# Optimization experiments

Hardware: AMD Instinct MI355X
Metric: run time of the kernel (lower is better)

## Reference

```python
import jax, jax.numpy as jnp
import numpy as np

FEATURES = 1024
NUM_REFLECTIONS = 4
BATCH = 65536


def setup_inputs() -> dict:
    key = jax.random.key(0)
    kx, kv = jax.random.split(key)
    x = jax.random.normal(kx, (BATCH, FEATURES), dtype=jnp.float32)
    vectors = jax.random.normal(kv, (NUM_REFLECTIONS, FEATURES), dtype=jnp.float32)
    return {"x": x, "vectors": vectors}


def _construct_orthogonal(vectors):
    n = vectors.shape[-1]
    I = jnp.eye(n, dtype=vectors.dtype)
    Q = I
    # Small fixed loop over reflections (num_reflections is tiny).
    for i in range(vectors.shape[0]):
        v = vectors[i]
        v = v / jnp.linalg.norm(v)  # F.normalize(v, dim=-1)
        H = I - 2.0 * jnp.outer(v, v)
        Q = H @ Q
    return Q


def reference(x, vectors):
    W = _construct_orthogonal(vectors)
    return x @ W.T
```

## Files before the change

kernel.cpp:

```cpp
#include <hip/hip_runtime.h>
#include <hip/hip_bf16.h>

#define FEATURES 1024
#define NREFL 4

__global__ __launch_bounds__(256) void hh_normalize(const float* __restrict__ vec,
                                                    float* __restrict__ w) {
    __shared__ float red[4];
    const int i = blockIdx.x;
    const int t = threadIdx.x;
    const float4 val = *(const float4*)(vec + i * FEATURES + t * 4);
    float s = val.x * val.x + val.y * val.y + val.z * val.z + val.w * val.w;
    #pragma unroll
    for (int off = 32; off > 0; off >>= 1) s += __shfl_xor(s, off);
    if ((t & 63) == 0) red[t >> 6] = s;
    __syncthreads();
    const float total = red[0] + red[1] + red[2] + red[3];
    const float inv = 1.0f / sqrtf(total);
    float4 o;
    o.x = val.x * inv; o.y = val.y * inv; o.z = val.z * inv; o.w = val.w * inv;
    *(float4*)(w + i * FEATURES + t * 4) = o;
}

__global__ __launch_bounds__(256) void hh_apply(const float* __restrict__ x,
                                                const float* __restrict__ w,
                                                float* __restrict__ out,
                                                int batch) {
    const int lane   = threadIdx.x & 63;
    const int wave   = blockIdx.x * (blockDim.x >> 6) + (threadIdx.x >> 6);
    const int nwaves = gridDim.x * (blockDim.x >> 6);

    float4 v[NREFL][4];
    #pragma unroll
    for (int i = 0; i < NREFL; ++i)
        #pragma unroll
        for (int c = 0; c < 4; ++c)
            v[i][c] = *(const float4*)(w + i * FEATURES + c * 256 + lane * 4);

    for (int row = wave; row < batch; row += nwaves) {
        const float* xr = x + (size_t)row * FEATURES;
        float4 y[4];
        #pragma unroll
        for (int c = 0; c < 4; ++c)
            y[c] = *(const float4*)(xr + c * 256 + lane * 4);

        #pragma unroll
        for (int i = 0; i < NREFL; ++i) {
            float d = 0.0f;
            #pragma unroll
            for (int c = 0; c < 4; ++c)
                d += y[c].x * v[i][c].x + y[c].y * v[i][c].y +
                     y[c].z * v[i][c].z + y[c].w * v[i][c].w;
            #pragma unroll
            for (int off = 32; off > 0; off >>= 1) d += __shfl_xor(d, off);
            d *= 2.0f;
            #pragma unroll
            for (int c = 0; c < 4; ++c) {
                y[c].x -= d * v[i][c].x;
                y[c].y -= d * v[i][c].y;
                y[c].z -= d * v[i][c].z;
                y[c].w -= d * v[i][c].w;
            }
        }

        float* orow = out + (size_t)row * FEATURES;
        #pragma unroll
        for (int c = 0; c < 4; ++c)
            *(float4*)(orow + c * 256 + lane * 4) = y[c];
    }
}

extern "C" void kernel_launch(void* const* d_in, const int* in_sizes, int n_in,
                              void* d_out, int out_size, void* d_ws, size_t ws_size,
                              hipStream_t stream) {
    const float* x   = (const float*)d_in[0];
    const float* vec = (const float*)d_in[1];
    float* out = (float*)d_out;
    float* wv  = (float*)d_ws;

    const int batch = in_sizes[0] / FEATURES;

    hh_normalize<<<NREFL, 256, 0, stream>>>(vec, wv);

    hh_apply<<<2048, 256, 0, stream>>>(x, wv, out, batch);
}
```

Measured before the change: 434.1 us.

## Fuse normalization into apply kernel, process two rows per wave, use nontemporal memory ops

Drops the separate normalize kernel: each wave loads the raw reflection vectors, computes their norms with wave shuffles and normalizes them in registers. The main loop now handles two rows per iteration so that more independent loads are in flight, and input loads and output stores use nontemporal hints to bypass cache retention. This removes one kernel launch and its dependency, at the cost of redundant per-wave norm computation and higher register pressure.

Result: faster. 423.1 us (-2.5%).

```diff
diff --git a/kernel.cpp b/kernel.cpp
--- a/kernel.cpp
+++ b/kernel.cpp
@@ -1,49 +1,90 @@
 #include <hip/hip_runtime.h>
-#include <hip/hip_bf16.h>
 
 #define FEATURES 1024
 #define NREFL 4
 
-__global__ __launch_bounds__(256) void hh_normalize(const float* __restrict__ vec,
-                                                    float* __restrict__ w) {
-    __shared__ float red[4];
-    const int i = blockIdx.x;
-    const int t = threadIdx.x;
-    const float4 val = *(const float4*)(vec + i * FEATURES + t * 4);
-    float s = val.x * val.x + val.y * val.y + val.z * val.z + val.w * val.w;
-    #pragma unroll
-    for (int off = 32; off > 0; off >>= 1) s += __shfl_xor(s, off);
-    if ((t & 63) == 0) red[t >> 6] = s;
-    __syncthreads();
-    const float total = red[0] + red[1] + red[2] + red[3];
-    const float inv = 1.0f / sqrtf(total);
-    float4 o;
-    o.x = val.x * inv; o.y = val.y * inv; o.z = val.z * inv; o.w = val.w * inv;
-    *(float4*)(w + i * FEATURES + t * 4) = o;
-}
+typedef float f32x4 __attribute__((ext_vector_type(4)));
 
-__global__ __launch_bounds__(256) void hh_apply(const float* __restrict__ x,
-                                                const float* __restrict__ w,
+__global__ __launch_bounds__(256) void hh_fused(const float* __restrict__ x,
+                                                const float* __restrict__ vec,
                                                 float* __restrict__ out,
                                                 int batch) {
     const int lane   = threadIdx.x & 63;
     const int wave   = blockIdx.x * (blockDim.x >> 6) + (threadIdx.x >> 6);
     const int nwaves = gridDim.x * (blockDim.x >> 6);
 
-    float4 v[NREFL][4];
+    f32x4 v[NREFL][4];
+    float s[NREFL];
     #pragma unroll
-    for (int i = 0; i < NREFL; ++i)
+    for (int i = 0; i < NREFL; ++i) {
+        s[i] = 0.0f;
+        #pragma unroll
+        for (int c = 0; c < 4; ++c) {
+            const f32x4 t = *(const f32x4*)(vec + i * FEATURES + c * 256 + lane * 4);
+            v[i][c] = t;
+            s[i] += t.x * t.x + t.y * t.y + t.z * t.z + t.w * t.w;
+        }
+    }
+    #pragma unroll
+    for (int off = 32; off > 0; off >>= 1) {
+        #pragma unroll
+        for (int i = 0; i < NREFL; ++i) s[i] += __shfl_xor(s[i], off);
+    }
+    #pragma unroll
+    for (int i = 0; i < NREFL; ++i) {
+        const float inv = 1.0f / sqrtf(s[i]);
+        #pragma unroll
+        for (int c = 0; c < 4; ++c) v[i][c] *= inv;
+    }
+
+    int row = wave;
+    for (; row + nwaves < batch; row += 2 * nwaves) {
+        const float* xr0 = x + (size_t)row * FEATURES;
+        const float* xr1 = x + ((size_t)row + nwaves) * FEATURES;
+        f32x4 ya[4], yb[4];
+        #pragma unroll
+        for (int c = 0; c < 4; ++c) {
+            ya[c] = __builtin_nontemporal_load((const f32x4*)(xr0 + c * 256 + lane * 4));
+            yb[c] = __builtin_nontemporal_load((const f32x4*)(xr1 + c * 256 + lane * 4));
+        }
+
+        #pragma unroll
+        for (int i = 0; i < NREFL; ++i) {
+            float da = 0.0f, db = 0.0f;
+            #pragma unroll
+            for (int c = 0; c < 4; ++c) {
+                da += ya[c].x * v[i][c].x + ya[c].y * v[i][c].y +
+                      ya[c].z * v[i][c].z + ya[c].w * v[i][c].w;
+                db += yb[c].x * v[i][c].x + yb[c].y * v[i][c].y +
+                      yb[c].z * v[i][c].z + yb[c].w * v[i][c].w;
+            }
+            #pragma unroll
+            for (int off = 32; off > 0; off >>= 1) {
+                da += __shfl_xor(da, off);
+                db += __shfl_xor(db, off);
+            }
+            da *= 2.0f; db *= 2.0f;
+            #pragma unroll
+            for (int c = 0; c < 4; ++c) {
+                ya[c] -= da * v[i][c];
+                yb[c] -= db * v[i][c];
+            }
+        }
+
+        float* o0 = out + (size_t)row * FEATURES;
+        float* o1 = out + ((size_t)row + nwaves) * FEATURES;
+        #pragma unroll
+        for (int c = 0; c < 4; ++c) {
+            __builtin_nontemporal_store(ya[c], (f32x4*)(o0 + c * 256 + lane * 4));
+            __builtin_nontemporal_store(yb[c], (f32x4*)(o1 + c * 256 + lane * 4));
+        }
+    }
+    for (; row < batch; row += nwaves) {
+        const float* xr = x + (size_t)row * FEATURES;
+        f32x4 y[4];
         #pragma unroll
         for (int c = 0; c < 4; ++c)
-            v[i][c] = *(const float4*)(w + i * FEATURES + c * 256 + lane * 4);
-
-    for (int row = wave; row < batch; row += nwaves) {
-        const float* xr = x + (size_t)row * FEATURES;
-        float4 y[4];
-        #pragma unroll
-        for (int c = 0; c < 4; ++c)
-            y[c] = *(const float4*)(xr + c * 256 + lane * 4);
-
+            y[c] = __builtin_nontemporal_load((const f32x4*)(xr + c * 256 + lane * 4));
         #pragma unroll
         for (int i = 0; i < NREFL; ++i) {
             float d = 0.0f;
@@ -55,18 +96,12 @@
             for (int off = 32; off > 0; off >>= 1) d += __shfl_xor(d, off);
             d *= 2.0f;
             #pragma unroll
-            for (int c = 0; c < 4; ++c) {
-                y[c].x -= d * v[i][c].x;
-                y[c].y -= d * v[i][c].y;
-                y[c].z -= d * v[i][c].z;
-                y[c].w -= d * v[i][c].w;
-            }
+            for (int c = 0; c < 4; ++c) y[c] -= d * v[i][c];
         }
-
         float* orow = out + (size_t)row * FEATURES;
         #pragma unroll
         for (int c = 0; c < 4; ++c)
-            *(float4*)(orow + c * 256 + lane * 4) = y[c];
+            __builtin_nontemporal_store(y[c], (f32x4*)(orow + c * 256 + lane * 4));
     }
 }
 
@@ -76,11 +111,8 @@
     const float* x   = (const float*)d_in[0];
     const float* vec = (const float*)d_in[1];
     float* out = (float*)d_out;
-    float* wv  = (float*)d_ws;
 
     const int batch = in_sizes[0] / FEATURES;
 
-    hh_normalize<<<NREFL, 256, 0, stream>>>(vec, wv);
-
-    hh_apply<<<2048, 256, 0, stream>>>(x, wv, out, batch);
+    hh_fused<<<2048, 256, 0, stream>>>(x, vec, out, batch);
 }
```
